# Kernel optimization log

Measured on AMD Instinct MI355X. Metric: run time of the kernel, lower is better.

## Reference

```python
import jax, jax.numpy as jnp
import numpy as np

D_MODEL = 1024
NUM_HEADS = 16
D_FF = 4096
MAX_SEQ_LEN = 2048
THETA = 10000.0
EPS = 1e-5
B, S = 2, 2048


def setup_inputs() -> dict:
    key = jax.random.key(0)
    ks = jax.random.split(key, 10)
    scale = 0.02
    inp = {
        "in_features": jax.random.normal(ks[0], (B, S, D_MODEL), dtype=jnp.float32),
        "token_positions": jnp.broadcast_to(jnp.arange(S, dtype=jnp.int32), (B, S)),
        "q_w": jax.random.normal(ks[1], (D_MODEL, D_MODEL), dtype=jnp.float32) * scale,
        "k_w": jax.random.normal(ks[2], (D_MODEL, D_MODEL), dtype=jnp.float32) * scale,
        "v_w": jax.random.normal(ks[3], (D_MODEL, D_MODEL), dtype=jnp.float32) * scale,
        "o_w": jax.random.normal(ks[4], (D_MODEL, D_MODEL), dtype=jnp.float32) * scale,
        "ln1_w": jnp.ones((D_MODEL,), dtype=jnp.float32),
        "ln2_w": jnp.ones((D_MODEL,), dtype=jnp.float32),
        "ffn_w1": jax.random.normal(ks[5], (D_FF, D_MODEL), dtype=jnp.float32) * scale,
        "ffn_w2": jax.random.normal(ks[6], (D_MODEL, D_FF), dtype=jnp.float32) * scale,
        "ffn_w3": jax.random.normal(ks[7], (D_FF, D_MODEL), dtype=jnp.float32) * scale,
    }
    return inp


def _rmsnorm(x, w, eps=EPS):
    return x * jax.lax.rsqrt(jnp.mean(x * x, axis=-1, keepdims=True) + eps) * w


def _rope(x, pos, theta=THETA):
    # x: [B, H, S, Dh]; pos: [B, S] int
    dh = x.shape[-1]
    inv_freq = theta ** (-jnp.arange(0, dh, 2, dtype=jnp.float32) / dh)  # [Dh/2]
    ang = pos.astype(jnp.float32)[..., None] * inv_freq                  # [B, S, Dh/2]
    cos = jnp.cos(ang)[:, None, :, :]  # [B, 1, S, Dh/2]
    sin = jnp.sin(ang)[:, None, :, :]
    x1, x2 = x[..., 0::2], x[..., 1::2]
    r1 = x1 * cos - x2 * sin
    r2 = x1 * sin + x2 * cos
    return jnp.stack([r1, r2], axis=-1).reshape(x.shape)


def _block(x, pos, q_w, k_w, v_w, o_w, ln1_w, ln2_w, w1, w2, w3):
    b, s, d = x.shape
    h, dh = NUM_HEADS, d // NUM_HEADS
    # Pre-LN attention
    xn = _rmsnorm(x, ln1_w)
    q = jnp.einsum('bsd,ed->bse', xn, q_w).reshape(b, s, h, dh).transpose(0, 2, 1, 3)
    k = jnp.einsum('bsd,ed->bse', xn, k_w).reshape(b, s, h, dh).transpose(0, 2, 1, 3)
    v = jnp.einsum('bsd,ed->bse', xn, v_w).reshape(b, s, h, dh).transpose(0, 2, 1, 3)
    q = _rope(q, pos)
    k = _rope(k, pos)
    scores = jnp.einsum('bhqd,bhkd->bhqk', q, k) / jnp.sqrt(jnp.float32(dh))
    causal = jnp.tril(jnp.ones((s, s), dtype=bool))
    scores = jnp.where(causal, scores, jnp.float32(-1e9))
    attn = jax.nn.softmax(scores, axis=-1)
    ctx = jnp.einsum('bhqk,bhkd->bhqd', attn, v).transpose(0, 2, 1, 3).reshape(b, s, d)
    attn_out = jnp.einsum('bsd,ed->bse', ctx, o_w)
    x = x + attn_out
    # Pre-LN SwiGLU FFN
    xn2 = _rmsnorm(x, ln2_w)
    g = jnp.einsum('bsd,fd->bsf', xn2, w1)
    u = jnp.einsum('bsd,fd->bsf', xn2, w3)
    ffn_out = jnp.einsum('bsf,df->bsd', jax.nn.silu(g) * u, w2)
    return x + ffn_out


def reference(in_features, token_positions, q_w, k_w, v_w, o_w, ln1_w, ln2_w, ffn_w1, ffn_w2, ffn_w3):
    return _block(in_features, token_positions, q_w, k_w, v_w, o_w, ln1_w, ln2_w, ffn_w1, ffn_w2, ffn_w3)
```

## Files before the change

### kernel.cpp

```cpp
#include <hip/hip_runtime.h>
#include <hip/hip_bf16.h>

typedef __attribute__((ext_vector_type(8))) __bf16 bf16x8;
typedef __attribute__((ext_vector_type(4))) float f32x4;

#define DEV static __device__ __forceinline__

DEV unsigned short f2bf(float f) {
  __bf16 h = (__bf16)f;
  union { __bf16 h; unsigned short u; } v; v.h = h;
  return v.u;
}
DEV float bf2f(unsigned short h) {
  union { unsigned int u; float f; } v; v.u = ((unsigned int)h) << 16;
  return v.f;
}
DEV unsigned pkbf(float lo, float hi) {
  union { __bf16 h[2]; unsigned u; } v;
  v.h[0] = (__bf16)lo; v.h[1] = (__bf16)hi;
  return v.u;
}
DEV f32x4 mfma16(bf16x8 a, bf16x8 b, f32x4 c) {
  return __builtin_amdgcn_mfma_f32_16x16x32_bf16(a, b, c, 0, 0, 0);
}
DEV void gload_lds16(const void* g, void* l) {
  __builtin_amdgcn_global_load_lds((__attribute__((address_space(1))) void*)g,
                                   (__attribute__((address_space(3))) void*)l,
                                   16, 0, 0);
}
DEV float fexp2(float x) { return exp2f(x); }

struct CvtArgs { const float* src[7]; int cum[8]; };
__global__ __launch_bounds__(256) void cvt_all(CvtArgs a, unsigned short* __restrict__ dst) {
  int i = (blockIdx.x * 256 + threadIdx.x) * 4;
  if (i >= a.cum[7]) return;
  int w = 0;
#pragma unroll 7
  for (int t = 0; t < 7; ++t) if (i >= a.cum[t + 1]) w = t + 1;
  float4 v = *(const float4*)(a.src[w] + (i - a.cum[w]));
  dst[i + 0] = f2bf(v.x);
  dst[i + 1] = f2bf(v.y);
  dst[i + 2] = f2bf(v.z);
  dst[i + 3] = f2bf(v.w);
}

__global__ __launch_bounds__(256) void rmsnorm_k(const float* __restrict__ x,
                                                 const float* __restrict__ w,
                                                 unsigned short* __restrict__ out) {
  int row = blockIdx.x;
  int tid = threadIdx.x;
  const float* xr = x + (size_t)row * 1024;
  float4 v = *(const float4*)(xr + tid * 4);
  float ss = v.x * v.x + v.y * v.y + v.z * v.z + v.w * v.w;
#pragma unroll
  for (int m = 32; m >= 1; m >>= 1) ss += __shfl_xor(ss, m);
  __shared__ float red[4];
  int wid = tid >> 6;
  if ((tid & 63) == 0) red[wid] = ss;
  __syncthreads();
  float tot = red[0] + red[1] + red[2] + red[3];
  float rs = rsqrtf(tot * (1.0f / 1024.0f) + 1e-5f);
  float4 wv = *(const float4*)(w + tid * 4);
  unsigned short* o = out + (size_t)row * 1024 + tid * 4;
  o[0] = f2bf(v.x * rs * wv.x);
  o[1] = f2bf(v.y * rs * wv.y);
  o[2] = f2bf(v.z * rs * wv.z);
  o[3] = f2bf(v.w * rs * wv.w);
}

__global__ __launch_bounds__(256) void rope2_k(unsigned short* __restrict__ q,
                                               unsigned short* __restrict__ k,
                                               const int* __restrict__ pos) {
  int idx = blockIdx.x * 256 + threadIdx.x;
  int i = idx & 31;
  int s = (idx >> 5) & 2047;
  int bh = idx >> 16;
  int b = bh >> 4;
  float p = (float)pos[b * 2048 + s];
  float inv = exp2f(-(float)i * 0.4152410118609203f);
  float ang = p * inv;
  float sn = sinf(ang), cs = cosf(ang);
  size_t base = (((size_t)bh * 2048) + s) * 64 + 2 * i;
  float q1 = bf2f(q[base]), q2 = bf2f(q[base + 1]);
  q[base]     = f2bf(q1 * cs - q2 * sn);
  q[base + 1] = f2bf(q1 * sn + q2 * cs);
  float k1 = bf2f(k[base]), k2 = bf2f(k[base + 1]);
  k[base]     = f2bf(k1 * cs - k2 * sn);
  k[base + 1] = f2bf(k1 * sn + k2 * cs);
}

template <int MODE>
DEV void gemm8_body(const unsigned short* __restrict__ A, int lda,
                    const unsigned short* __restrict__ B, int ldb,
                    int bm, int bn, int kbase, int nt,
                    unsigned short* __restrict__ outb, float* __restrict__ outf,
                    const float* __restrict__ resid, const unsigned short* __restrict__ gate,
                    unsigned short* As, unsigned short* Bs) {
  const int tid = threadIdx.x;
  const int lane = tid & 63, wid = tid >> 6;
  const int wr = wid >> 2, wc = wid & 3;
  const int m0 = bm * 256, n0 = bn * 256;

  const int r0 = tid >> 2, r1 = 128 + (tid >> 2), cc = tid & 3;
  const int sc0 = (cc ^ ((r0 >> 1) & 3)) * 8;
  const int sc1 = (cc ^ ((r1 >> 1) & 3)) * 8;
  const size_t arow0 = (size_t)(m0 + r0) * lda, arow1 = (size_t)(m0 + r1) * lda;
  const size_t brow0 = (size_t)(n0 + r0) * ldb, brow1 = (size_t)(n0 + r1) * ldb;
  const int du0 = tid * 8, du1 = (512 + tid) * 8;

  auto stA = [&](int t, int kh) {
    unsigned short* d = As + ((((t & 1) << 1) | kh) * 8192);
    const unsigned short* s = A + kbase + t * 64 + kh * 32;
    gload_lds16(s + arow0 + sc0, d + du0);
    gload_lds16(s + arow1 + sc1, d + du1);
  };
  auto stB = [&](int t, int kh) {
    unsigned short* d = Bs + ((((t & 1) << 1) | kh) * 8192);
    const unsigned short* s = B + kbase + t * 64 + kh * 32;
    gload_lds16(s + brow0 + sc0, d + du0);
    gload_lds16(s + brow1 + sc1, d + du1);
  };

  const int fcol = ((lane >> 4) ^ ((lane >> 1) & 3)) * 8;
  const int frow = lane & 15;
  const int abase = (wr * 128 + frow) * 32 + fcol;
  const int bbase = (wc * 64 + frow) * 32 + fcol;

  f32x4 acc[8][4] = {};
  bf16x8 a[4], b[4];

#define LOADA(buf, ks, mh) { const unsigned short* p_ = As + (((buf) << 1) | (ks)) * 8192 + abase + (mh) * 2048; \
  a[0] = *(const bf16x8*)(p_); a[1] = *(const bf16x8*)(p_ + 512); \
  a[2] = *(const bf16x8*)(p_ + 1024); a[3] = *(const bf16x8*)(p_ + 1536); }
#define LOADB(buf, ks) { const unsigned short* p_ = Bs + (((buf) << 1) | (ks)) * 8192 + bbase; \
  b[0] = *(const bf16x8*)(p_); b[1] = *(const bf16x8*)(p_ + 512); \
  b[2] = *(const bf16x8*)(p_ + 1024); b[3] = *(const bf16x8*)(p_ + 1536); }
#define MFMAQ(mh) { _Pragma("unroll") for (int fi = 0; fi < 4; ++fi) \
  _Pragma("unroll") for (int j = 0; j < 4; ++j) \
    acc[(mh) * 4 + fi][j] = mfma16(a[fi], b[j], acc[(mh) * 4 + fi][j]); }
#define LGK0() { asm volatile("s_waitcnt lgkmcnt(0)" ::: "memory"); __builtin_amdgcn_sched_barrier(0); }

  stA(0, 0); stB(0, 0); stA(0, 1); stB(0, 1);
  stA(1, 0); stB(1, 0);
  asm volatile("s_waitcnt vmcnt(4)" ::: "memory");
  __builtin_amdgcn_s_barrier();

  for (int t = 0; t < nt; ++t) {
    const int buf = t & 1;
    LOADA(buf, 0, 0); LOADB(buf, 0);
    if (t + 1 < nt) stA(t + 1, 1);
    __builtin_amdgcn_s_barrier();
    LGK0();
    __builtin_amdgcn_s_setprio(1); MFMAQ(0); __builtin_amdgcn_s_setprio(0);
    __builtin_amdgcn_s_barrier();
    LOADA(buf, 0, 1);
    if (t + 1 < nt) stB(t + 1, 1);
    __builtin_amdgcn_s_barrier();
    LGK0();
    __builtin_amdgcn_s_setprio(1); MFMAQ(1); __builtin_amdgcn_s_setprio(0);
    __builtin_amdgcn_s_barrier();
    LOADA(buf, 1, 0); LOADB(buf, 1);
    if (t + 2 < nt) stA(t + 2, 0);
    __builtin_amdgcn_s_barrier();
    LGK0();
    __builtin_amdgcn_s_setprio(1); MFMAQ(0); __builtin_amdgcn_s_setprio(0);
    __builtin_amdgcn_s_barrier();
    LOADA(buf, 1, 1);
    if (t + 2 < nt) stB(t + 2, 0);
    __builtin_amdgcn_s_barrier();
    LGK0();
    __builtin_amdgcn_s_setprio(1); MFMAQ(1); __builtin_amdgcn_s_setprio(0);
    if (t + 1 < nt) {
      if (t + 2 < nt) { asm volatile("s_waitcnt vmcnt(4)" ::: "memory"); }
      else            { asm volatile("s_waitcnt vmcnt(0)" ::: "memory"); }
      __builtin_amdgcn_s_barrier();
    }
  }
#undef LOADA
#undef LOADB
#undef MFMAQ
#undef LGK0

#pragma unroll
  for (int i = 0; i < 8; ++i)
#pragma unroll
    for (int j = 0; j < 4; ++j)
#pragma unroll
      for (int r = 0; r < 4; ++r) {
        int m = m0 + wr * 128 + i * 16 + ((lane >> 4) << 2) + r;
        int n = n0 + wc * 64 + j * 16 + (lane & 15);
        float v = acc[i][j][r];
        if (MODE == 0) {
          unsigned short* dst = outb + ((n >= 1024) ? 4194304 : 0);
          int nn = n & 1023;
          int bb = m >> 11, s = m & 2047, hh = nn >> 6, dd = nn & 63;
          dst[(((size_t)bb * 16 + hh) * 2048 + s) * 64 + dd] = f2bf(v);
        } else if (MODE == 1) {
          int hh = m >> 6, dd = m & 63, bb = n >> 11, s = n & 2047;
          outb[(((size_t)bb * 16 + hh) * 64 + dd) * 2048 + s] = f2bf(v);
        } else if (MODE == 2) {
          size_t idx = (size_t)m * 1024 + n;
          outf[idx] = resid[idx] + v;
        } else if (MODE == 3) {
          outb[(size_t)m * 4096 + n] = f2bf(v);
        } else {
          size_t idx = (size_t)m * 4096 + n;
          float g = bf2f(gate[idx]);
          outb[idx] = f2bf(g / (1.0f + __expf(-g)) * v);
        }
      }
}

DEV void swz_map(int bid, int nwg, int MT, int& bm, int& bn) {
  int cpx = nwg >> 3;
  int sw = (bid & 7) * cpx + (bid >> 3);
  bm = sw % MT;
  bn = sw / MT;
}

template <int MODE>
__global__ __launch_bounds__(512, 2) void gemm8_k(const unsigned short* __restrict__ A, int lda,
                                                  const unsigned short* __restrict__ B, int ldb,
                                                  int MT, int nt,
                                                  unsigned short* __restrict__ outb,
                                                  float* __restrict__ outf,
                                                  const float* __restrict__ resid,
                                                  const unsigned short* __restrict__ gate) {
  __shared__ __align__(16) unsigned short lds[65536];
  int bm, bn;
  swz_map(blockIdx.x, gridDim.x, MT, bm, bn);
  gemm8_body<MODE>(A, lda, B, ldb, bm, bn, 0, nt, outb, outf, resid, gate, lds, lds + 32768);
}

__global__ __launch_bounds__(512, 2) void gemm8_qkv(const unsigned short* __restrict__ xn,
                                                    const unsigned short* __restrict__ wqk,
                                                    const unsigned short* __restrict__ wv,
                                                    unsigned short* __restrict__ qk_out,
                                                    unsigned short* __restrict__ vt_out) {
  __shared__ __align__(16) unsigned short lds[65536];
  int bid = blockIdx.x;
  if (bid < 128) {
    int bm, bn;
    swz_map(bid, 128, 16, bm, bn);
    gemm8_body<0>(xn, 1024, wqk, 1024, bm, bn, 0, 16, qk_out, nullptr, nullptr, nullptr, lds, lds + 32768);
  } else {
    bid -= 128;
    int bm, bn;
    swz_map(bid, 64, 4, bm, bn);
    gemm8_body<1>(wv, 1024, xn, 1024, bm, bn, 0, 16, vt_out, nullptr, nullptr, nullptr, lds, lds + 32768);
  }
}

template <int K>
__global__ __launch_bounds__(256) void gemm_res(const unsigned short* __restrict__ A,
                                                const unsigned short* __restrict__ Bw,
                                                float* __restrict__ outf,
                                                const float* __restrict__ resid) {
  __shared__ __align__(16) unsigned short As[128 * 64];
  __shared__ __align__(16) unsigned short Bs[128 * 64];
  const int N = 1024;
  const int tid = threadIdx.x;
  const int wid = tid >> 6, lane = tid & 63;
  const int wr = wid >> 1, wc = wid & 1;
  const int m0 = blockIdx.x * 128, n0 = blockIdx.y * 128;
  const int sw = (lane & 7) * 8;
  f32x4 acc[4][4] = {};

  for (int k0 = 0; k0 < K; k0 += 64) {
    __syncthreads();
#pragma unroll
    for (int it = 0; it < 4; ++it) {
      int c = wid * 4 + it;
      int row = c * 8 + (lane >> 3);
      int col = ((lane & 7) ^ (row & 7)) * 8;
      gload_lds16(A + (size_t)(m0 + row) * K + k0 + col, As + c * 512);
      gload_lds16(Bw + (size_t)(n0 + row) * K + k0 + col, Bs + c * 512);
    }
    asm volatile("s_waitcnt vmcnt(0)" ::: "memory");
    __syncthreads();
#pragma unroll
    for (int kk = 0; kk < 2; ++kk) {
      const int kof = (kk * 32 + (lane >> 4) * 8) ^ sw;
      bf16x8 af[4], bfr[4];
#pragma unroll
      for (int i = 0; i < 4; ++i) {
        af[i]  = *(const bf16x8*)(As + (wr * 64 + i * 16 + (lane & 15)) * 64 + kof);
        bfr[i] = *(const bf16x8*)(Bs + (wc * 64 + i * 16 + (lane & 15)) * 64 + kof);
      }
#pragma unroll
      for (int i = 0; i < 4; ++i)
#pragma unroll
        for (int j = 0; j < 4; ++j) acc[i][j] = mfma16(af[i], bfr[j], acc[i][j]);
    }
  }
  const int rb = m0 + wr * 64 + ((lane >> 4) * 4);
  const int cb = n0 + wc * 64 + (lane & 15);
#pragma unroll
  for (int i = 0; i < 4; ++i)
#pragma unroll
    for (int r = 0; r < 4; ++r) {
      int m = rb + i * 16 + r;
#pragma unroll
      for (int j = 0; j < 4; ++j) {
        size_t idx = (size_t)m * N + cb + j * 16;
        outf[idx] = resid[idx] + acc[i][j][r];
      }
    }
}

__global__ __launch_bounds__(256) void attn_k(const unsigned short* __restrict__ q,
                                              const unsigned short* __restrict__ k,
                                              const unsigned short* __restrict__ vt,
                                              unsigned short* __restrict__ ctx) {
  __shared__ __align__(16) unsigned short Ks[2][4096];
  __shared__ __align__(16) unsigned short Vs[2][4096];
  __shared__ __align__(16) unsigned short Ps[4][16 * 72];
  const int bid = blockIdx.x;
  const int bh = (bid & 7) * 4 + ((bid >> 3) & 3);
  const int qt = 31 - (bid >> 5);
  const int tid = threadIdx.x, wid = tid >> 6, lane = tid & 63;
  const size_t bhS = (size_t)bh * 2048;
  const size_t bhD = (size_t)bh * 64 * 2048;
  const int b = bh >> 4, hh = bh & 15;
  const int sw = (lane & 7) * 8;
  const int h4 = lane >> 4, l15 = lane & 15;
  const float SC2 = 0.18033688011112042f;

  const int c0 = wid * 2, c1 = wid * 2 + 1;
  const int row0 = c0 * 8 + (lane >> 3), row1 = c1 * 8 + (lane >> 3);
  const int col0 = ((lane & 7) ^ (row0 & 7)) * 8;
  const int col1 = ((lane & 7) ^ (row1 & 7)) * 8;

  auto stage = [&](int kt, int buf) {
    gload_lds16(k + (bhS + kt * 64 + row0) * 64 + col0, &Ks[buf][c0 * 512]);
    gload_lds16(k + (bhS + kt * 64 + row1) * 64 + col1, &Ks[buf][c1 * 512]);
    gload_lds16(vt + bhD + (size_t)row0 * 2048 + kt * 64 + col0, &Vs[buf][c0 * 512]);
    gload_lds16(vt + bhD + (size_t)row1 * 2048 + kt * 64 + col1, &Vs[buf][c1 * 512]);
  };

  const int q0 = qt * 64;
  bf16x8 qf[2];
  {
    const unsigned short* qp = q + (bhS + q0 + wid * 16 + l15) * 64 + h4 * 8;
    qf[0] = *(const bf16x8*)qp;
    qf[1] = *(const bf16x8*)(qp + 32);
#pragma unroll
    for (int jj = 0; jj < 8; ++jj) {
      qf[0][jj] = (__bf16)((float)qf[0][jj] * SC2);
      qf[1][jj] = (__bf16)((float)qf[1][jj] * SC2);
    }
  }
  float mrow = -1e30f, lrow = 0.0f;
  f32x4 o[4] = {};
  const int qg = q0 + wid * 16 + l15;
  const int rowb = q0 + wid * 16 + (h4 << 2);

  stage(0, 0);
  if (qt > 0) { stage(1, 1); asm volatile("s_waitcnt vmcnt(4)" ::: "memory"); }
  else        {              asm volatile("s_waitcnt vmcnt(0)" ::: "memory"); }
  __builtin_amdgcn_s_barrier();

  for (int kt = 0; kt <= qt; ++kt) {
    const int cur = kt & 1;
    float s[16];
#pragma unroll
    for (int nt = 0; nt < 4; ++nt) {
      f32x4 z = {};
#pragma unroll
      for (int ks = 0; ks < 2; ++ks) {
        int kof = (ks * 32 + h4 * 8) ^ sw;
        bf16x8 kf = *(const bf16x8*)(&Ks[cur][(nt * 16 + l15) * 64 + kof]);
        z = mfma16(kf, qf[ks], z);
      }
      s[nt * 4 + 0] = z[0]; s[nt * 4 + 1] = z[1];
      s[nt * 4 + 2] = z[2]; s[nt * 4 + 3] = z[3];
    }
    if (kt == qt) {
#pragma unroll
      for (int nt = 0; nt < 4; ++nt)
#pragma unroll
        for (int r = 0; r < 4; ++r) {
          int key = q0 + nt * 16 + (h4 << 2) + r;
          if (key > qg) s[nt * 4 + r] = -3e38f;
        }
    }
    float pmax = s[0];
#pragma unroll
    for (int i = 1; i < 16; ++i) pmax = fmaxf(pmax, s[i]);
    pmax = fmaxf(pmax, __shfl_xor(pmax, 16));
    pmax = fmaxf(pmax, __shfl_xor(pmax, 32));
    if (!__all(pmax <= mrow + 11.5f)) {
      float mnew = fmaxf(mrow, pmax);
      float dl = mrow - mnew;
      mrow = mnew;
      lrow *= fexp2(dl);
#pragma unroll
      for (int r = 0; r < 4; ++r) {
        float ar = fexp2(__shfl(dl, (h4 << 2) + r, 16));
#pragma unroll
        for (int d = 0; d < 4; ++d) o[d][r] *= ar;
      }
    }
    float sum = 0.0f;
#pragma unroll
    for (int i = 0; i < 16; ++i) { s[i] = fexp2(s[i] - mrow); sum += s[i]; }
    lrow += sum;
    {
      unsigned short* pr = &Ps[wid][l15 * 72 + (h4 << 2)];
#pragma unroll
      for (int nt = 0; nt < 4; ++nt) {
        uint2 w;
        w.x = pkbf(s[4 * nt], s[4 * nt + 1]);
        w.y = pkbf(s[4 * nt + 2], s[4 * nt + 3]);
        *(uint2*)(pr + nt * 16) = w;
      }
    }
#pragma unroll
    for (int ks = 0; ks < 2; ++ks) {
      bf16x8 pf = *(const bf16x8*)(&Ps[wid][l15 * 72 + ks * 32 + (h4 << 3)]);
      int kof = (ks * 32 + h4 * 8) ^ sw;
#pragma unroll
      for (int d = 0; d < 4; ++d) {
        bf16x8 vf = *(const bf16x8*)(&Vs[cur][(d * 16 + l15) * 64 + kof]);
        o[d] = mfma16(pf, vf, o[d]);
      }
    }
    __builtin_amdgcn_s_barrier();
    if (kt + 2 <= qt) {
      stage(kt + 2, cur);
      asm volatile("s_waitcnt vmcnt(4)" ::: "memory");
    } else if (kt + 1 <= qt) {
      asm volatile("s_waitcnt vmcnt(0)" ::: "memory");
    }
    __builtin_amdgcn_s_barrier();
  }
  lrow += __shfl_xor(lrow, 16);
  lrow += __shfl_xor(lrow, 32);
  float inv = 1.0f / lrow;
#pragma unroll
  for (int r = 0; r < 4; ++r) {
    float invr = __shfl(inv, (h4 << 2) + r, 16);
#pragma unroll
    for (int d = 0; d < 4; ++d)
      ctx[((size_t)b * 2048 + (rowb + r)) * 1024 + hh * 64 + d * 16 + l15] = f2bf(o[d][r] * invr);
  }
}

extern "C" void kernel_launch(void* const* d_in, const int* in_sizes, int n_in,
                              void* d_out, int out_size, void* d_ws, size_t ws_size,
                              hipStream_t stream) {
  (void)in_sizes; (void)n_in; (void)out_size; (void)ws_size;
  const float* in_f = (const float*)d_in[0];
  const int* pos    = (const int*)d_in[1];
  const float* q_w  = (const float*)d_in[2];
  const float* k_w  = (const float*)d_in[3];
  const float* v_w  = (const float*)d_in[4];
  const float* o_w  = (const float*)d_in[5];
  const float* ln1  = (const float*)d_in[6];
  const float* ln2  = (const float*)d_in[7];
  const float* w1   = (const float*)d_in[8];
  const float* w2   = (const float*)d_in[9];
  const float* w3   = (const float*)d_in[10];
  float* out = (float*)d_out;

  unsigned short* ws = (unsigned short*)d_ws;
  unsigned short* wb   = ws;
  unsigned short* wqkb = wb;
  unsigned short* wvb  = wb + 2097152;
  unsigned short* wob  = wb + 3145728;
  unsigned short* w1b  = wb + 4194304;
  unsigned short* w2b  = wb + 8388608;
  unsigned short* w3b  = wb + 12582912;
  unsigned short* xn   = ws + 16777216;
  unsigned short* qb   = ws + 20971520;
  unsigned short* kb   = ws + 25165824;
  unsigned short* vb   = ws + 29360128;
  unsigned short* cx   = ws + 33554432;
  unsigned short* gb   = ws + 37748736;
  unsigned short* hb   = ws + 54525952;

  CvtArgs ca;
  ca.src[0] = q_w; ca.src[1] = k_w; ca.src[2] = v_w; ca.src[3] = o_w;
  ca.src[4] = w1;  ca.src[5] = w2;  ca.src[6] = w3;
  ca.cum[0] = 0;        ca.cum[1] = 1048576;  ca.cum[2] = 2097152;  ca.cum[3] = 3145728;
  ca.cum[4] = 4194304;  ca.cum[5] = 8388608;  ca.cum[6] = 12582912; ca.cum[7] = 16777216;
  cvt_all<<<16384, 256, 0, stream>>>(ca, wb);

  rmsnorm_k<<<4096, 256, 0, stream>>>(in_f, ln1, xn);

  gemm8_qkv<<<192, 512, 0, stream>>>(xn, wqkb, wvb, qb, vb);

  rope2_k<<<8192, 256, 0, stream>>>(qb, kb, pos);

  attn_k<<<1024, 256, 0, stream>>>(qb, kb, vb, cx);

  gemm_res<1024><<<dim3(32, 8), 256, 0, stream>>>(cx, wob, out, in_f);

  rmsnorm_k<<<4096, 256, 0, stream>>>(out, ln2, xn);

  gemm8_k<3><<<256, 512, 0, stream>>>(xn, 1024, w1b, 1024, 16, 16, gb, nullptr, nullptr, nullptr);
  gemm8_k<4><<<256, 512, 0, stream>>>(xn, 1024, w3b, 1024, 16, 16, hb, nullptr, nullptr, gb);

  gemm_res<4096><<<dim3(32, 8), 256, 0, stream>>>(hb, w2b, out, out);
}
```

Before: 294.1 us.

## Split-K the FFN down-projection over big-tile GEMM with a reduction kernel

Replaces the gemm_res<4096> down-projection with the 256x256-tile gemm8 kernel run as a 4-way split-K (grid 64x4). Each K slice writes fp32 partials into workspace, and a new reduce_k kernel adds the four partials to the residual in place. The aim is better MFMA tile efficiency and enough workgroups to fill the GPU for the K=4096 GEMM. The cost is 64 MB of extra partial-sum traffic plus one more kernel launch.

```diff
diff --git a/kernel.cpp b/kernel.cpp
--- a/kernel.cpp
+++ b/kernel.cpp
@@ -203,10 +203,12 @@
           outf[idx] = resid[idx] + v;
         } else if (MODE == 3) {
           outb[(size_t)m * 4096 + n] = f2bf(v);
-        } else {
+        } else if (MODE == 4) {
           size_t idx = (size_t)m * 4096 + n;
           float g = bf2f(gate[idx]);
           outb[idx] = f2bf(g / (1.0f + __expf(-g)) * v);
+        } else {
+          outf[(size_t)m * 1024 + n] = v;
         }
       }
 }
@@ -221,7 +223,7 @@
 template <int MODE>
 __global__ __launch_bounds__(512, 2) void gemm8_k(const unsigned short* __restrict__ A, int lda,
                                                   const unsigned short* __restrict__ B, int ldb,
-                                                  int MT, int nt,
+                                                  int MT, int kz, int nt,
                                                   unsigned short* __restrict__ outb,
                                                   float* __restrict__ outf,
                                                   const float* __restrict__ resid,
@@ -229,7 +231,10 @@
   __shared__ __align__(16) unsigned short lds[65536];
   int bm, bn;
   swz_map(blockIdx.x, gridDim.x, MT, bm, bn);
-  gemm8_body<MODE>(A, lda, B, ldb, bm, bn, 0, nt, outb, outf, resid, gate, lds, lds + 32768);
+  int kb = kz * blockIdx.y;
+  float* of = outf;
+  if (MODE == 5) of += (size_t)blockIdx.y * 4194304;
+  gemm8_body<MODE>(A, lda, B, ldb, bm, bn, kb, nt, outb, of, resid, gate, lds, lds + 32768);
 }
 
 __global__ __launch_bounds__(512, 2) void gemm8_qkv(const unsigned short* __restrict__ xn,
@@ -308,6 +313,21 @@
     }
 }
 
+__global__ __launch_bounds__(256) void reduce_k(float* __restrict__ out,
+                                                const float* __restrict__ part) {
+  int i = (blockIdx.x * 256 + threadIdx.x) * 4;
+  float4 o = *(const float4*)(out + i);
+  float4 p0 = *(const float4*)(part + i);
+  float4 p1 = *(const float4*)(part + 4194304 + i);
+  float4 p2 = *(const float4*)(part + 8388608 + i);
+  float4 p3 = *(const float4*)(part + 12582912 + i);
+  o.x += p0.x + p1.x + p2.x + p3.x;
+  o.y += p0.y + p1.y + p2.y + p3.y;
+  o.z += p0.z + p1.z + p2.z + p3.z;
+  o.w += p0.w + p1.w + p2.w + p3.w;
+  *(float4*)(out + i) = o;
+}
+
 __global__ __launch_bounds__(256) void attn_k(const unsigned short* __restrict__ q,
                                               const unsigned short* __restrict__ k,
                                               const unsigned short* __restrict__ vt,
@@ -477,6 +497,7 @@
   unsigned short* vb   = ws + 29360128;
   unsigned short* cx   = ws + 33554432;
   unsigned short* gb   = ws + 37748736;
+  float* part          = (float*)(ws + 20971520);
   unsigned short* hb   = ws + 54525952;
 
   CvtArgs ca;
@@ -498,8 +519,9 @@
 
   rmsnorm_k<<<4096, 256, 0, stream>>>(out, ln2, xn);
 
-  gemm8_k<3><<<256, 512, 0, stream>>>(xn, 1024, w1b, 1024, 16, 16, gb, nullptr, nullptr, nullptr);
-  gemm8_k<4><<<256, 512, 0, stream>>>(xn, 1024, w3b, 1024, 16, 16, hb, nullptr, nullptr, gb);
-
-  gemm_res<4096><<<dim3(32, 8), 256, 0, stream>>>(hb, w2b, out, out);
-}
+  gemm8_k<3><<<256, 512, 0, stream>>>(xn, 1024, w1b, 1024, 16, 0, 16, gb, nullptr, nullptr, nullptr);
+  gemm8_k<4><<<256, 512, 0, stream>>>(xn, 1024, w3b, 1024, 16, 0, 16, hb, nullptr, nullptr, gb);
+  gemm8_k<5><<<dim3(64, 4), 512, 0, stream>>>(hb, 4096, w2b, 4096, 16, 1024, 16, nullptr, part, nullptr, nullptr);
+
+  reduce_k<<<4096, 256, 0, stream>>>(out, part);
+}
```

Result: faster. 283.6 us (-3.6%).

## Fuse W1/W3 GEMMs via interleaved weights and split-K the W2 GEMM

Applied to the files above, without the earlier changes.

Weights w1 and w3 are converted into one interleaved bf16 matrix, so a single 256x256-tile GEMM computes gate and up columns side by side. The SwiGLU is applied in the epilogue by pairing adjacent lanes with a shuffle, which removes the intermediate gate buffer and its re-read. The down projection now runs on the large-tile GEMM with 4-way split-K, writing bf16 partials that a separate reduce kernel adds into the residual output. This trades an extra launch, partial-sum traffic and bf16 rounding of the partials for better occupancy and fewer passes over memory.

```diff
diff --git a/kernel.cpp b/kernel.cpp
--- a/kernel.cpp
+++ b/kernel.cpp
@@ -37,11 +37,16 @@
   int w = 0;
 #pragma unroll 7
   for (int t = 0; t < 7; ++t) if (i >= a.cum[t + 1]) w = t + 1;
-  float4 v = *(const float4*)(a.src[w] + (i - a.cum[w]));
-  dst[i + 0] = f2bf(v.x);
-  dst[i + 1] = f2bf(v.y);
-  dst[i + 2] = f2bf(v.z);
-  dst[i + 3] = f2bf(v.w);
+  int local = i - a.cum[w];
+  int di;
+  if (w == 5)      di = 8388608 + ((local >> 10) << 11) + (local & 1023);
+  else if (w == 6) di = 8388608 + ((local >> 10) << 11) + 1024 + (local & 1023);
+  else             di = i;
+  float4 v = *(const float4*)(a.src[w] + local);
+  dst[di + 0] = f2bf(v.x);
+  dst[di + 1] = f2bf(v.y);
+  dst[di + 2] = f2bf(v.z);
+  dst[di + 3] = f2bf(v.w);
 }
 
 __global__ __launch_bounds__(256) void rmsnorm_k(const float* __restrict__ x,
@@ -94,7 +99,7 @@
                     const unsigned short* __restrict__ B, int ldb,
                     int bm, int bn, int kbase, int nt,
                     unsigned short* __restrict__ outb, float* __restrict__ outf,
-                    const float* __restrict__ resid, const unsigned short* __restrict__ gate,
+                    const float* __restrict__ resid,
                     unsigned short* As, unsigned short* Bs) {
   const int tid = threadIdx.x;
   const int lane = tid & 63, wid = tid >> 6;
@@ -201,12 +206,14 @@
         } else if (MODE == 2) {
           size_t idx = (size_t)m * 1024 + n;
           outf[idx] = resid[idx] + v;
-        } else if (MODE == 3) {
-          outb[(size_t)m * 4096 + n] = f2bf(v);
+        } else if (MODE == 5) {
+          outb[(size_t)m * 1024 + n] = f2bf(v);
         } else {
-          size_t idx = (size_t)m * 4096 + n;
-          float g = bf2f(gate[idx]);
-          outb[idx] = f2bf(g / (1.0f + __expf(-g)) * v);
+          float other = __shfl_xor(v, 1);
+          if (!(lane & 1)) {
+            float hv = v / (1.0f + __expf(-v)) * other;
+            outb[(size_t)m * 4096 + (n >> 1)] = f2bf(hv);
+          }
         }
       }
 }
@@ -221,15 +228,17 @@
 template <int MODE>
 __global__ __launch_bounds__(512, 2) void gemm8_k(const unsigned short* __restrict__ A, int lda,
                                                   const unsigned short* __restrict__ B, int ldb,
-                                                  int MT, int nt,
+                                                  int MT, int kz, int nt,
                                                   unsigned short* __restrict__ outb,
                                                   float* __restrict__ outf,
-                                                  const float* __restrict__ resid,
-                                                  const unsigned short* __restrict__ gate) {
+                                                  const float* __restrict__ resid) {
   __shared__ __align__(16) unsigned short lds[65536];
   int bm, bn;
   swz_map(blockIdx.x, gridDim.x, MT, bm, bn);
-  gemm8_body<MODE>(A, lda, B, ldb, bm, bn, 0, nt, outb, outf, resid, gate, lds, lds + 32768);
+  int kb = kz * blockIdx.y;
+  unsigned short* ob = outb;
+  if (MODE == 5) ob += (size_t)blockIdx.y * 4194304;
+  gemm8_body<MODE>(A, lda, B, ldb, bm, bn, kb, nt, ob, outf, resid, lds, lds + 32768);
 }
 
 __global__ __launch_bounds__(512, 2) void gemm8_qkv(const unsigned short* __restrict__ xn,
@@ -242,12 +251,12 @@
   if (bid < 128) {
     int bm, bn;
     swz_map(bid, 128, 16, bm, bn);
-    gemm8_body<0>(xn, 1024, wqk, 1024, bm, bn, 0, 16, qk_out, nullptr, nullptr, nullptr, lds, lds + 32768);
+    gemm8_body<0>(xn, 1024, wqk, 1024, bm, bn, 0, 16, qk_out, nullptr, nullptr, lds, lds + 32768);
   } else {
     bid -= 128;
     int bm, bn;
     swz_map(bid, 64, 4, bm, bn);
-    gemm8_body<1>(wv, 1024, xn, 1024, bm, bn, 0, 16, vt_out, nullptr, nullptr, nullptr, lds, lds + 32768);
+    gemm8_body<1>(wv, 1024, xn, 1024, bm, bn, 0, 16, vt_out, nullptr, nullptr, lds, lds + 32768);
   }
 }
 
@@ -306,6 +315,21 @@
         outf[idx] = resid[idx] + acc[i][j][r];
       }
     }
+}
+
+__global__ __launch_bounds__(256) void reduce_k(float* __restrict__ out,
+                                                const unsigned short* __restrict__ partb) {
+  int i = (blockIdx.x * 256 + threadIdx.x) * 4;
+  float4 o = *(const float4*)(out + i);
+#pragma unroll
+  for (int s = 0; s < 4; ++s) {
+    uint2 w = *(const uint2*)(partb + (size_t)s * 4194304 + i);
+    o.x += bf2f((unsigned short)(w.x & 0xffff));
+    o.y += bf2f((unsigned short)(w.x >> 16));
+    o.z += bf2f((unsigned short)(w.y & 0xffff));
+    o.w += bf2f((unsigned short)(w.y >> 16));
+  }
+  *(float4*)(out + i) = o;
 }
 
 __global__ __launch_bounds__(256) void attn_k(const unsigned short* __restrict__ q,
@@ -468,20 +492,19 @@
   unsigned short* wqkb = wb;
   unsigned short* wvb  = wb + 2097152;
   unsigned short* wob  = wb + 3145728;
-  unsigned short* w1b  = wb + 4194304;
-  unsigned short* w2b  = wb + 8388608;
-  unsigned short* w3b  = wb + 12582912;
+  unsigned short* w2b  = wb + 4194304;
+  unsigned short* w13b = wb + 8388608;
   unsigned short* xn   = ws + 16777216;
   unsigned short* qb   = ws + 20971520;
   unsigned short* kb   = ws + 25165824;
   unsigned short* vb   = ws + 29360128;
   unsigned short* cx   = ws + 33554432;
-  unsigned short* gb   = ws + 37748736;
+  unsigned short* partb = ws + 20971520;
   unsigned short* hb   = ws + 54525952;
 
   CvtArgs ca;
   ca.src[0] = q_w; ca.src[1] = k_w; ca.src[2] = v_w; ca.src[3] = o_w;
-  ca.src[4] = w1;  ca.src[5] = w2;  ca.src[6] = w3;
+  ca.src[4] = w2;  ca.src[5] = w1;  ca.src[6] = w3;
   ca.cum[0] = 0;        ca.cum[1] = 1048576;  ca.cum[2] = 2097152;  ca.cum[3] = 3145728;
   ca.cum[4] = 4194304;  ca.cum[5] = 8388608;  ca.cum[6] = 12582912; ca.cum[7] = 16777216;
   cvt_all<<<16384, 256, 0, stream>>>(ca, wb);
@@ -498,8 +521,9 @@
 
   rmsnorm_k<<<4096, 256, 0, stream>>>(out, ln2, xn);
 
-  gemm8_k<3><<<256, 512, 0, stream>>>(xn, 1024, w1b, 1024, 16, 16, gb, nullptr, nullptr, nullptr);
-  gemm8_k<4><<<256, 512, 0, stream>>>(xn, 1024, w3b, 1024, 16, 16, hb, nullptr, nullptr, gb);
-
-  gemm_res<4096><<<dim3(32, 8), 256, 0, stream>>>(hb, w2b, out, out);
-}
+  gemm8_k<6><<<512, 512, 0, stream>>>(xn, 1024, w13b, 1024, 16, 0, 16, hb, nullptr, nullptr);
+
+  gemm8_k<5><<<dim3(64, 4), 512, 0, stream>>>(hb, 4096, w2b, 4096, 16, 1024, 16, partb, nullptr, nullptr);
+
+  reduce_k<<<4096, 256, 0, stream>>>(out, partb);
+}
```

After: 282.2 us. 1.04x faster.
